# Kernel tuning notes

Measured on AMD Instinct MI355X. Metric: run time of the kernel, lower is better.

## Reference

```python
import jax, jax.numpy as jnp
import numpy as np
from jax import lax

BEV_SIZE = 250
BEV_RANGE = 50.0
BEV_RES = 0.4
SZ = BEV_SIZE * BEV_SIZE
N_POINTS = 5_000_000
EPS = 1e-5


def setup_inputs() -> dict:
    key = jax.random.key(0)
    ks = jax.random.split(key, 8)
    # points: x,y in [-55,55) (some out of range), z in [-3,5), intensity in [0,1)
    xy = jax.random.uniform(ks[0], (N_POINTS, 2), jnp.float32, -55.0, 55.0)
    z = jax.random.uniform(ks[1], (N_POINTS, 1), jnp.float32, -3.0, 5.0)
    it = jax.random.uniform(ks[2], (N_POINTS, 1), jnp.float32, 0.0, 1.0)
    points = jnp.concatenate([xy, z, it], axis=1)

    def he(k, shape):
        fan_in = shape[1] * shape[2] * shape[3]
        return jax.random.normal(k, shape, jnp.float32) * np.sqrt(2.0 / fan_in)

    return {
        "points": points,
        "w1": he(ks[3], (32, 4, 3, 3)), "b1": jnp.zeros(32), "g1": jnp.ones(32), "beta1": jnp.zeros(32),
        "w2": he(ks[4], (64, 32, 3, 3)), "b2": jnp.zeros(64), "g2": jnp.ones(64), "beta2": jnp.zeros(64),
        "w3": he(ks[5], (64, 64, 3, 3)), "b3": jnp.zeros(64), "g3": jnp.ones(64), "beta3": jnp.zeros(64),
    }


def points_to_bev(points):
    x, y, z, inten = points[:, 0], points[:, 1], points[:, 2], points[:, 3]
    valid = (x >= -BEV_RANGE) & (x < BEV_RANGE) & (y >= -BEV_RANGE) & (y < BEV_RANGE)
    xi = jnp.clip(((x + BEV_RANGE) / BEV_RES).astype(jnp.int32), 0, BEV_SIZE - 1)
    yi = jnp.clip(((y + BEV_RANGE) / BEV_RES).astype(jnp.int32), 0, BEV_SIZE - 1)
    # invalid points routed to an extra dummy bin SZ, sliced off afterwards
    flat = jnp.where(valid, yi * BEV_SIZE + xi, SZ)

    max_z = jnp.full(SZ + 1, -jnp.inf, jnp.float32).at[flat].max(z)[:SZ]
    max_z = jnp.where(jnp.isinf(max_z), 0.0, max_z)
    min_z = jnp.full(SZ + 1, jnp.inf, jnp.float32).at[flat].min(z)[:SZ]
    min_z = jnp.where(jnp.isinf(min_z), 0.0, min_z)
    density = jnp.zeros(SZ + 1, jnp.float32).at[flat].add(1.0)[:SZ]
    isum = jnp.zeros(SZ + 1, jnp.float32).at[flat].add(inten)[:SZ]
    mean_i = jnp.where(density > 0, isum / jnp.maximum(density, 1.0), 0.0)

    bev = jnp.stack([max_z, min_z, jnp.log1p(density), mean_i], axis=0)
    return bev.reshape(4, BEV_SIZE, BEV_SIZE)


def conv_bn_relu(x, w, b, g, beta):
    # x: (1, Cin, H, W), w: (Cout, Cin, 3, 3)
    y = lax.conv_general_dilated(x, w, (1, 1), "SAME",
                                 dimension_numbers=("NCHW", "OIHW", "NCHW"))
    y = y + b[None, :, None, None]
    # BatchNorm2d in training mode: batch stats over (N, H, W)
    mu = jnp.mean(y, axis=(0, 2, 3), keepdims=True)
    var = jnp.mean((y - mu) ** 2, axis=(0, 2, 3), keepdims=True)
    y = (y - mu) * lax.rsqrt(var + EPS)
    y = y * g[None, :, None, None] + beta[None, :, None, None]
    return jax.nn.relu(y)


def reference(points, w1, b1, g1, beta1, w2, b2, g2, beta2, w3, b3, g3, beta3):
    bev = points_to_bev(points)[None]  # (1, 4, 250, 250)
    h = conv_bn_relu(bev, w1, b1, g1, beta1)
    h = conv_bn_relu(h, w2, b2, g2, beta2)
    h = conv_bn_relu(h, w3, b3, g3, beta3)
    return h  # (1, 64, 250, 250)
```

## Files before the change

### kernel.cpp

```cpp
#include <hip/hip_runtime.h>


constexpr int BEVW = 250;
constexpr int SZC  = BEVW * BEVW;
constexpr int NB   = 512;
constexpr int PPT  = 16;
constexpr int CHUNK = 256 * PPT;
constexpr int NBKT = 100;
constexpr int NCELL = 625;
constexpr int CAPB = 43008;
constexpr int NTILE = 256;

__device__ __forceinline__ unsigned f2ord(float f) {
    unsigned u = __float_as_uint(f);
    return (u & 0x80000000u) ? ~u : (u | 0x80000000u);
}
__device__ __forceinline__ float ord2f(unsigned u) {
    unsigned b = (u & 0x80000000u) ? (u & 0x7FFFFFFFu) : ~u;
    return __uint_as_float(b);
}

__global__ void k_initg(unsigned* __restrict__ gcnt) {
    if (threadIdx.x < 128) gcnt[threadIdx.x] = 0u;
}

__launch_bounds__(256)
__global__ void k_bucket(const float4* __restrict__ pts, int n,
                         unsigned long long* __restrict__ recs,
                         unsigned* __restrict__ gcnt) {
    __shared__ unsigned lcnt[NBKT];
    __shared__ unsigned lbase[NBKT];
    const int tid = threadIdx.x;
    if (tid < NBKT) lcnt[tid] = 0u;
    __syncthreads();

    const int ppb = (n + NB - 1) / NB;
    const int start = blockIdx.x * ppb;
    const int end = min(start + ppb, n);

    for (int c0 = start; c0 < end; c0 += CHUNK) {
        unsigned long long rec[PPT];
        int bkt[PPT];
        unsigned slot[PPT];
        unsigned vmask = 0u;
#pragma unroll
        for (int k = 0; k < PPT; ++k) {
            int p = c0 + k * 256 + tid;
            if (p >= end) continue;
            float4 q = pts[p];
            if (!(q.x >= -50.0f && q.x < 50.0f && q.y >= -50.0f && q.y < 50.0f))
                continue;
            int xi = (int)((q.x + 50.0f) / 0.4f);
            int yi = (int)((q.y + 50.0f) / 0.4f);
            xi = min(max(xi, 0), BEVW - 1);
            yi = min(max(yi, 0), BEVW - 1);
            int b  = (yi / 25) * 10 + (xi / 25);
            int cl = (yi % 25) * 25 + (xi % 25);
            unsigned iq = (unsigned)(q.w * 4194304.0f);
            rec[k] = ((unsigned long long)f2ord(q.z) << 32) |
                     ((unsigned long long)(unsigned)cl << 22) | iq;
            bkt[k] = b;
            slot[k] = atomicAdd(&lcnt[b], 1u);
            vmask |= 1u << k;
        }
        __syncthreads();
        if (tid < NBKT) {
            unsigned c = lcnt[tid];
            if (c) lbase[tid] = atomicAdd(&gcnt[tid], c);
            lcnt[tid] = 0u;
        }
        __syncthreads();
#pragma unroll
        for (int k = 0; k < PPT; ++k) {
            if (!((vmask >> k) & 1u)) continue;
            unsigned idx = lbase[bkt[k]] + slot[k];
            if (idx < (unsigned)CAPB)
                recs[(size_t)bkt[k] * CAPB + idx] = rec[k];
        }
    }
}

__launch_bounds__(1024)
__global__ void k_reduce(const unsigned long long* __restrict__ recs,
                         const unsigned* __restrict__ gcnt,
                         float* __restrict__ bev) {
    __shared__ unsigned mxA[NCELL], mnA[NCELL], ctA[NCELL], siA[NCELL];
    const int b = blockIdx.x;
    for (int i = threadIdx.x; i < NCELL; i += 1024) {
        mxA[i] = 0u; mnA[i] = 0xFFFFFFFFu; ctA[i] = 0u; siA[i] = 0u;
    }
    __syncthreads();
    const unsigned nb = min(gcnt[b], (unsigned)CAPB);
    const unsigned long long* rb = recs + (size_t)b * CAPB;
    for (unsigned i = threadIdx.x; i < nb; i += 1024) {
        unsigned long long r = rb[i];
        unsigned zo = (unsigned)(r >> 32);
        unsigned cl = ((unsigned)(r >> 22)) & 0x3FFu;
        unsigned iq = (unsigned)r & 0x3FFFFFu;
        atomicMax(&mxA[cl], zo);
        atomicMin(&mnA[cl], zo);
        atomicAdd(&ctA[cl], 1u);
        atomicAdd(&siA[cl], iq);
    }
    __syncthreads();
    const int tx = b % 10, ty = b / 10;
    for (int i = threadIdx.x; i < NCELL; i += 1024) {
        int cy = ty * 25 + i / 25, cx = tx * 25 + i % 25;
        int cell = cy * BEVW + cx;
        unsigned c = ctA[i];
        bool has = c > 0u;
        float dn = (float)c;
        float isum = (float)siA[i] * (1.0f / 4194304.0f);
        bev[0 * SZC + cell] = has ? ord2f(mxA[i]) : 0.0f;
        bev[1 * SZC + cell] = has ? ord2f(mnA[i]) : 0.0f;
        bev[2 * SZC + cell] = log1pf(dn);
        bev[3 * SZC + cell] = has ? isum / dn : 0.0f;
    }
}

__global__ void k_wt(const float* __restrict__ w, float* __restrict__ wt,
                     int CIN, int COUT) {
    int i = blockIdx.x * blockDim.x + threadIdx.x;
    if (i >= COUT * CIN * 9) return;
    int oc = i / (CIN * 9);
    int r  = i % (CIN * 9);
    int ic = r / 9, k = r % 9;
    wt[(ic * 9 + k) * COUT + oc] = w[i];
}

template <int CIN, int COUT, int ICB, int OCG, bool FUSE>
__launch_bounds__(256, 8)
__global__ void k_conv(const float* __restrict__ in, const float* __restrict__ wt,
                       const float* __restrict__ bias, const float* __restrict__ ab,
                       float* __restrict__ out, double* __restrict__ bnpart) {
    __shared__ float s_in[ICB][18 * 18];
    __shared__ double s_red[4][OCG][2];

    const int tid = threadIdx.x;
    const int u = tid & 15, v = tid >> 4;
    const int tile = blockIdx.x;
    const int tx = (tile & 15) * 16, ty = (tile >> 4) * 16;
    const int oc0 = blockIdx.y * OCG;
    const int lane = tid & 63, wid = tid >> 6;

    float acc[OCG];
#pragma unroll
    for (int o = 0; o < OCG; ++o) acc[o] = 0.0f;

    for (int ic0 = 0; ic0 < CIN; ic0 += ICB) {
        __syncthreads();
        for (int e = tid; e < ICB * 324; e += 256) {
            int c = e / 324, rem = e % 324;
            int r = rem / 18, q = rem % 18;
            int cg = ic0 + c;
            int gy = ty - 1 + r, gx = tx - 1 + q;
            float x = 0.0f;
            if (gy >= 0 && gy < BEVW && gx >= 0 && gx < BEVW) {
                x = in[(size_t)cg * SZC + gy * BEVW + gx];
                if (FUSE) x = fmaxf(fmaf(x, ab[2 * cg], ab[2 * cg + 1]), 0.0f);
            }
            s_in[c][rem] = x;
        }
        __syncthreads();

#pragma unroll
        for (int icl = 0; icl < ICB; ++icl) {
            const int icg = ic0 + icl;
#pragma unroll
            for (int tap = 0; tap < 9; ++tap) {
                const int ky = tap / 3, kx = tap % 3;
                float x = s_in[icl][(v + ky) * 18 + u + kx];
                const float* wk = wt + ((size_t)(icg * 9 + tap) * COUT + oc0);
#pragma unroll
                for (int o = 0; o < OCG; ++o)
                    acc[o] = fmaf(x, wk[o], acc[o]);
            }
        }
    }

    const int ox = tx + u, oy = ty + v;
    const bool valid = (ox < BEVW) && (oy < BEVW);
#pragma unroll
    for (int o = 0; o < OCG; ++o) {
        float y = acc[o] + bias[oc0 + o];
        if (valid) out[(size_t)(oc0 + o) * SZC + oy * BEVW + ox] = y;
        double s = valid ? (double)y : 0.0;
        double s2 = valid ? (double)y * (double)y : 0.0;
#pragma unroll
        for (int off = 32; off; off >>= 1) {
            s  += __shfl_down(s, off);
            s2 += __shfl_down(s2, off);
        }
        if (lane == 0) { s_red[wid][o][0] = s; s_red[wid][o][1] = s2; }
    }
    __syncthreads();
    if (tid < OCG) {
        double S = 0.0, S2 = 0.0;
#pragma unroll
        for (int wv = 0; wv < 4; ++wv) { S += s_red[wv][tid][0]; S2 += s_red[wv][tid][1]; }
        bnpart[((size_t)(oc0 + tid) * NTILE + tile) * 2]     = S;
        bnpart[((size_t)(oc0 + tid) * NTILE + tile) * 2 + 1] = S2;
    }
}

__global__ void k_bnstats2(const double* __restrict__ part, const float* __restrict__ g,
                           const float* __restrict__ beta, float* __restrict__ statsAB) {
    int c = threadIdx.x;
    double S = 0.0, S2 = 0.0;
    for (int t = 0; t < NTILE; ++t) {
        S  += part[((size_t)c * NTILE + t) * 2];
        S2 += part[((size_t)c * NTILE + t) * 2 + 1];
    }
    double mu  = S / (double)SZC;
    double var = S2 / (double)SZC - mu * mu;
    double A = (1.0 / sqrt(var + 1e-5)) * (double)g[c];
    statsAB[2 * c]     = (float)A;
    statsAB[2 * c + 1] = (float)((double)beta[c] - mu * A);
}

__global__ void k_bnreluS(const float* __restrict__ y, const float* __restrict__ ab,
                          float* __restrict__ out) {
    int c = blockIdx.y;
    int i = blockIdx.x * blockDim.x + threadIdx.x;
    if (i >= SZC) return;
    size_t idx = (size_t)c * SZC + i;
    out[idx] = fmaxf(fmaf(y[idx], ab[2 * c], ab[2 * c + 1]), 0.0f);
}

extern "C" void kernel_launch(void* const* d_in, const int* in_sizes, int n_in,
                              void* d_out, int out_size, void* d_ws, size_t ws_size,
                              hipStream_t stream) {
    const float4* pts = (const float4*)d_in[0];
    const float* w1 = (const float*)d_in[1];
    const float* b1 = (const float*)d_in[2];
    const float* g1 = (const float*)d_in[3];
    const float* be1 = (const float*)d_in[4];
    const float* w2 = (const float*)d_in[5];
    const float* b2 = (const float*)d_in[6];
    const float* g2 = (const float*)d_in[7];
    const float* be2 = (const float*)d_in[8];
    const float* w3 = (const float*)d_in[9];
    const float* b3 = (const float*)d_in[10];
    const float* g3 = (const float*)d_in[11];
    const float* be3 = (const float*)d_in[12];

    float* ws = (float*)d_ws;
    const size_t wsf = ws_size / 4;

    constexpr size_t TAILF = 128 + 250000 + 64 + 128 + 128 + 65536 + 1152 + 18432 + 36864;
    float* tail = ws + (wsf - TAILF);
    unsigned* gcnt = (unsigned*)tail;
    float* bev = tail + 128;
    float* st1 = bev + 4 * SZC;
    float* st2 = st1 + 64;
    float* st3 = st2 + 128;
    double* bnpart = (double*)(st3 + 128);
    float* wt1 = st3 + 128 + 65536;
    float* wt2 = wt1 + 1152;
    float* wt3 = wt2 + 18432;

    unsigned long long* recs = (unsigned long long*)ws;
    float* y1 = ws;
    float* y2 = ws + 2000000;
    float* out = (float*)d_out;

    int n = in_sizes[0] / 4;
    const int cellBlocks = (SZC + 255) / 256;

    k_wt<<<(32 * 4 * 9 + 255) / 256, 256, 0, stream>>>(w1, wt1, 4, 32);
    k_wt<<<(64 * 32 * 9 + 255) / 256, 256, 0, stream>>>(w2, wt2, 32, 64);
    k_wt<<<(64 * 64 * 9 + 255) / 256, 256, 0, stream>>>(w3, wt3, 64, 64);

    k_initg<<<1, 128, 0, stream>>>(gcnt);
    k_bucket<<<NB, 256, 0, stream>>>(pts, n, recs, gcnt);
    k_reduce<<<NBKT, 1024, 0, stream>>>(recs, gcnt, bev);

    k_conv<4, 32, 4, 8, false><<<dim3(NTILE, 4), 256, 0, stream>>>(bev, wt1, b1, nullptr, y1, bnpart);
    k_bnstats2<<<1, 32, 0, stream>>>(bnpart, g1, be1, st1);

    k_conv<32, 64, 8, 8, true><<<dim3(NTILE, 8), 256, 0, stream>>>(y1, wt2, b2, st1, y2, bnpart);
    k_bnstats2<<<1, 64, 0, stream>>>(bnpart, g2, be2, st2);

    k_conv<64, 64, 8, 8, true><<<dim3(NTILE, 8), 256, 0, stream>>>(y2, wt3, b3, st2, out, bnpart);
    k_bnstats2<<<1, 64, 0, stream>>>(bnpart, g3, be3, st3);

    k_bnreluS<<<dim3(cellBlocks, 64), 256, 0, stream>>>(out, st3, out);
}
```

Baseline: 327.5 us.

## Double-buffer conv input tiles via register prefetch and widen output-channel group

The conv kernel now double-buffers the shared-memory input halo, loading the next channel block into registers while the current one is computed, then storing it to the other buffer. This hides global-load latency and removes one barrier per iteration. Rows are padded to a 19-float stride to cut LDS bank conflicts. OCG doubles from 8 to 16 so each input tile is reused across more output channels and half as many blocks reload it. Launch bounds no longer force 8 waves per SIMD, which risks more register pressure and lower occupancy.

```diff
diff --git a/kernel.cpp b/kernel.cpp
--- a/kernel.cpp
+++ b/kernel.cpp
@@ -129,11 +129,16 @@
 }
 
 template <int CIN, int COUT, int ICB, int OCG, bool FUSE>
-__launch_bounds__(256, 8)
+__launch_bounds__(256)
 __global__ void k_conv(const float* __restrict__ in, const float* __restrict__ wt,
                        const float* __restrict__ bias, const float* __restrict__ ab,
                        float* __restrict__ out, double* __restrict__ bnpart) {
-    __shared__ float s_in[ICB][18 * 18];
+    constexpr int PH = CIN / ICB;
+    constexpr int RS = 19;
+    constexpr int CSZ = 18 * RS;
+    constexpr int TE = ICB * 324;
+    constexpr int NJ = (TE + 255) / 256;
+    __shared__ float s_in[2][ICB][CSZ];
     __shared__ double s_red[4][OCG][2];
 
     const int tid = threadIdx.x;
@@ -147,35 +152,73 @@
 #pragma unroll
     for (int o = 0; o < OCG; ++o) acc[o] = 0.0f;
 
-    for (int ic0 = 0; ic0 < CIN; ic0 += ICB) {
-        __syncthreads();
-        for (int e = tid; e < ICB * 324; e += 256) {
+#pragma unroll
+    for (int j = 0; j < NJ; ++j) {
+        int e = j * 256 + tid;
+        if (e < TE) {
             int c = e / 324, rem = e % 324;
             int r = rem / 18, q = rem % 18;
-            int cg = ic0 + c;
             int gy = ty - 1 + r, gx = tx - 1 + q;
             float x = 0.0f;
             if (gy >= 0 && gy < BEVW && gx >= 0 && gx < BEVW) {
-                x = in[(size_t)cg * SZC + gy * BEVW + gx];
-                if (FUSE) x = fmaxf(fmaf(x, ab[2 * cg], ab[2 * cg + 1]), 0.0f);
+                x = in[(size_t)c * SZC + gy * BEVW + gx];
+                if (FUSE) x = fmaxf(fmaf(x, ab[2 * c], ab[2 * c + 1]), 0.0f);
             }
-            s_in[c][rem] = x;
-        }
-        __syncthreads();
+            s_in[0][c][r * RS + q] = x;
+        }
+    }
+    __syncthreads();
+
+#pragma unroll 1
+    for (int t = 0; t < PH; ++t) {
+        const int cur = t & 1;
+
+        float rv[NJ];
+        if (t + 1 < PH) {
+            const int icn = (t + 1) * ICB;
+#pragma unroll
+            for (int j = 0; j < NJ; ++j) {
+                int e = j * 256 + tid;
+                rv[j] = 0.0f;
+                if (e < TE) {
+                    int c = e / 324, rem = e % 324;
+                    int r = rem / 18, q = rem % 18;
+                    int gy = ty - 1 + r, gx = tx - 1 + q;
+                    if (gy >= 0 && gy < BEVW && gx >= 0 && gx < BEVW) {
+                        int cg = icn + c;
+                        float x = in[(size_t)cg * SZC + gy * BEVW + gx];
+                        if (FUSE) x = fmaxf(fmaf(x, ab[2 * cg], ab[2 * cg + 1]), 0.0f);
+                        rv[j] = x;
+                    }
+                }
+            }
+        }
 
 #pragma unroll
         for (int icl = 0; icl < ICB; ++icl) {
-            const int icg = ic0 + icl;
+            const int icg = t * ICB + icl;
 #pragma unroll
             for (int tap = 0; tap < 9; ++tap) {
                 const int ky = tap / 3, kx = tap % 3;
-                float x = s_in[icl][(v + ky) * 18 + u + kx];
+                float x = s_in[cur][icl][(v + ky) * RS + u + kx];
                 const float* wk = wt + ((size_t)(icg * 9 + tap) * COUT + oc0);
 #pragma unroll
                 for (int o = 0; o < OCG; ++o)
                     acc[o] = fmaf(x, wk[o], acc[o]);
             }
         }
+
+        if (t + 1 < PH) {
+#pragma unroll
+            for (int j = 0; j < NJ; ++j) {
+                int e = j * 256 + tid;
+                if (e < TE) {
+                    int c = e / 324, rem = e % 324;
+                    s_in[cur ^ 1][c][(rem / 18) * RS + rem % 18] = rv[j];
+                }
+            }
+        }
+        __syncthreads();
     }
 
     const int ox = tx + u, oy = ty + v;
@@ -275,13 +318,13 @@
     k_bucket<<<NB, 256, 0, stream>>>(pts, n, recs, gcnt);
     k_reduce<<<NBKT, 1024, 0, stream>>>(recs, gcnt, bev);
 
-    k_conv<4, 32, 4, 8, false><<<dim3(NTILE, 4), 256, 0, stream>>>(bev, wt1, b1, nullptr, y1, bnpart);
+    k_conv<4, 32, 4, 16, false><<<dim3(NTILE, 2), 256, 0, stream>>>(bev, wt1, b1, nullptr, y1, bnpart);
     k_bnstats2<<<1, 32, 0, stream>>>(bnpart, g1, be1, st1);
 
-    k_conv<32, 64, 8, 8, true><<<dim3(NTILE, 8), 256, 0, stream>>>(y1, wt2, b2, st1, y2, bnpart);
+    k_conv<32, 64, 8, 16, true><<<dim3(NTILE, 4), 256, 0, stream>>>(y1, wt2, b2, st1, y2, bnpart);
     k_bnstats2<<<1, 64, 0, stream>>>(bnpart, g2, be2, st2);
 
-    k_conv<64, 64, 8, 8, true><<<dim3(NTILE, 8), 256, 0, stream>>>(y2, wt3, b3, st2, out, bnpart);
+    k_conv<64, 64, 8, 16, true><<<dim3(NTILE, 4), 256, 0, stream>>>(y2, wt3, b3, st2, out, bnpart);
     k_bnstats2<<<1, 64, 0, stream>>>(bnpart, g3, be3, st3);
 
     k_bnreluS<<<dim3(cellBlocks, 64), 256, 0, stream>>>(out, st3, out);
```

After: 819.9 us. 150% more time.
